# Optimization experiments

Measured on AMD Instinct MI355X. Metric: run time of the kernel, lower is better.

Reference implementation:

```python
import jax, jax.numpy as jnp
import numpy as np

N, E, IN_CH, EDGE_DIM, OUT_CH = 50000, 600000, 128, 64, 128


def setup_inputs() -> dict:
    key = jax.random.key(0)
    ks = jax.random.split(key, 9)
    return {
        "x": jax.random.normal(ks[0], (N, IN_CH), dtype=jnp.float32),
        "edge_index": jax.random.randint(ks[1], (2, E), 0, N, dtype=jnp.int64),
        "edge_attr": jax.random.normal(ks[2], (E, EDGE_DIM), dtype=jnp.float32),
        "Wx": jax.random.normal(ks[3], (IN_CH, OUT_CH), dtype=jnp.float32) * 0.05,
        "bx": jax.random.normal(ks[4], (OUT_CH,), dtype=jnp.float32) * 0.05,
        "We": jax.random.normal(ks[5], (EDGE_DIM, OUT_CH), dtype=jnp.float32) * 0.05,
        "be": jax.random.normal(ks[6], (OUT_CH,), dtype=jnp.float32) * 0.05,
        "Wm": jax.random.normal(ks[7], (2 * OUT_CH, OUT_CH), dtype=jnp.float32) * 0.05,
        "bm": jax.random.normal(ks[8], (OUT_CH,), dtype=jnp.float32) * 0.05,
        "beta": jnp.float32(0.1),
    }


def reference(x, edge_index, edge_attr, Wx, bx, We, be, Wm, bm, beta):
    # node / edge projections
    xp = x @ Wx + bx                      # [N, out]
    ef = edge_attr @ We + be              # [E, out]
    src, dst = edge_index[0], edge_index[1]
    # gather source node features, combine with edge features
    msg = jnp.concatenate([xp[src], ef], axis=1)   # [E, 2*out]
    msg = jax.nn.leaky_relu(msg @ Wm + bm)         # slope 0.01 matches torch default
    # scatter-add into destination nodes
    agg = jax.ops.segment_sum(msg, dst, num_segments=xp.shape[0])  # [N, out]
    return jax.nn.sigmoid(agg) * jax.nn.relu(beta)
```

## Files before the change

kernel.cpp:

```cpp
#include <hip/hip_runtime.h>


#define NB 25000
#define NB_SHIFT 1
#define TPW 4

typedef __bf16 bf16x8 __attribute__((ext_vector_type(8)));
typedef float  f32x4  __attribute__((ext_vector_type(4)));
typedef unsigned short ushort_t;
typedef unsigned int   uint_t;

__device__ __forceinline__ ushort_t f2b(float f) {
    uint_t u = __float_as_uint(f);
    u += 0x7FFF + ((u >> 16) & 1);
    return (ushort_t)(u >> 16);
}
__device__ __forceinline__ uint_t pack2(float a, float b) {
    return (uint_t)f2b(a) | ((uint_t)f2b(b) << 16);
}

__global__ void fuse_weights_kernel(const float* __restrict__ Wx,
                                    const float* __restrict__ bx,
                                    const float* __restrict__ We,
                                    const float* __restrict__ be,
                                    const float* __restrict__ Wm,
                                    const float* __restrict__ bm,
                                    ushort_t* __restrict__ WxmT16,
                                    ushort_t* __restrict__ WemT16,
                                    float* __restrict__ bf) {
    int idx = blockIdx.x * blockDim.x + threadIdx.x;
    if (idx < 128 * 128) {
        int r = idx >> 7, c = idx & 127;
        float acc = 0.f;
        #pragma unroll 8
        for (int j = 0; j < 128; ++j) acc += Wx[r * 128 + j] * Wm[j * 128 + c];
        WxmT16[c * 128 + r] = f2b(acc);
    } else if (idx < 128 * 128 + 64 * 128) {
        int t = idx - 128 * 128;
        int r = t >> 7, c = t & 127;
        float acc = 0.f;
        #pragma unroll 8
        for (int j = 0; j < 128; ++j) acc += We[r * 128 + j] * Wm[(128 + j) * 128 + c];
        WemT16[c * 64 + r] = f2b(acc);
    } else if (idx < 128 * 128 + 64 * 128 + 128) {
        int c = idx - (128 * 128 + 64 * 128);
        float acc = bm[c];
        #pragma unroll 8
        for (int j = 0; j < 128; ++j)
            acc += bx[j] * Wm[j * 128 + c] + be[j] * Wm[(128 + j) * 128 + c];
        bf[c] = acc;
    }
}

__global__ __launch_bounds__(256) void node_gemm_kernel(
        const float* __restrict__ x, const ushort_t* __restrict__ WxmT16,
        const float* __restrict__ bf, ushort_t* __restrict__ ub, int N) {
    int tid = threadIdx.x;
    int g = blockIdx.x * 4 + (tid >> 6);
    if (g >= (N / 16) * 2) return;
    int lane = tid & 63, l15 = lane & 15, quad = lane >> 4;
    int n0 = (g >> 1) * 16;
    int chBase = (g & 1) * 64;

    bf16x8 B[4][4];
    #pragma unroll
    for (int ct = 0; ct < 4; ++ct)
        #pragma unroll
        for (int kk = 0; kk < 4; ++kk)
            B[ct][kk] = __builtin_bit_cast(bf16x8, *((const uint4*)
                &WxmT16[(size_t)(chBase + ct * 16 + l15) * 128 + kk * 32 + quad * 8]));

    bf16x8 A[4];
    #pragma unroll
    for (int kk = 0; kk < 4; ++kk) {
        const float4* s = (const float4*)&x[(size_t)(n0 + l15) * 128 + kk * 32 + quad * 8];
        float4 v0 = s[0], v1 = s[1];
        uint4 w;
        w.x = pack2(v0.x, v0.y);
        w.y = pack2(v0.z, v0.w);
        w.z = pack2(v1.x, v1.y);
        w.w = pack2(v1.z, v1.w);
        A[kk] = __builtin_bit_cast(bf16x8, w);
    }

    f32x4 acc[4] = {{0.f,0.f,0.f,0.f},{0.f,0.f,0.f,0.f},
                    {0.f,0.f,0.f,0.f},{0.f,0.f,0.f,0.f}};
    #pragma unroll
    for (int kk = 0; kk < 4; ++kk)
        #pragma unroll
        for (int ct = 0; ct < 4; ++ct)
            acc[ct] = __builtin_amdgcn_mfma_f32_16x16x32_bf16(B[ct][kk], A[kk], acc[ct], 0, 0, 0);

    #pragma unroll
    for (int ct = 0; ct < 4; ++ct) {
        int ch = chBase + ct * 16 + quad * 4;
        float4 bv = *(const float4*)&bf[ch];
        uint2 w;
        w.x = pack2(acc[ct][0] + bv.x, acc[ct][1] + bv.y);
        w.y = pack2(acc[ct][2] + bv.z, acc[ct][3] + bv.w);
        *((uint2*)&ub[(size_t)(n0 + l15) * 128 + ch]) = w;
    }
}

__global__ __launch_bounds__(1024) void hist_kernel(
        const int* __restrict__ ei, int* __restrict__ cnt, int E) {
    __shared__ int lcnt[NB];
    int t = threadIdx.x;
    for (int i = t; i < NB; i += 1024) lcnt[i] = 0;
    __syncthreads();
    int base = blockIdx.x * 16384;
    #pragma unroll
    for (int j = 0; j < 16; ++j) {
        int e = base + t + j * 1024;
        if (e < E) atomicAdd(&lcnt[ei[E + e] >> NB_SHIFT], 1);
    }
    __syncthreads();
    for (int i = t; i < NB; i += 1024) {
        int c = lcnt[i];
        if (c) atomicAdd(&cnt[i], c);
    }
}

__global__ __launch_bounds__(1024) void scan_kernel(
        const int* __restrict__ cnt, int* __restrict__ start,
        int* __restrict__ cur, int nb, int E) {
    __shared__ int tot[1024];
    int t = threadIdx.x;
    int v[25]; int sum = 0;
    #pragma unroll
    for (int j = 0; j < 25; ++j) {
        int i = t * 25 + j;
        v[j] = (i < nb) ? cnt[i] : 0;
        sum += v[j];
    }
    tot[t] = sum;
    __syncthreads();
    for (int d = 1; d < 1024; d <<= 1) {
        int val = tot[t];
        int add = (t >= d) ? tot[t - d] : 0;
        __syncthreads();
        tot[t] = val + add;
        __syncthreads();
    }
    int ex = (t == 0) ? 0 : tot[t - 1];
    #pragma unroll
    for (int j = 0; j < 25; ++j) {
        int i = t * 25 + j;
        if (i < nb) { start[i] = ex; cur[i] = ex; }
        ex += v[j];
    }
    if (t == 1023) start[nb] = ex;
}

__global__ __launch_bounds__(1024) void binpos_kernel(
        const int* __restrict__ ei, int* __restrict__ cur,
        int* __restrict__ pos, uint_t* __restrict__ recs, int E) {
    __shared__ int lcnt[NB];
    int t = threadIdx.x;
    for (int i = t; i < NB; i += 1024) lcnt[i] = 0;
    __syncthreads();
    int base = blockIdx.x * 16384;
    int myrank[16], mybkt[16];
    #pragma unroll
    for (int j = 0; j < 16; ++j) {
        int e = base + t + j * 1024;
        if (e < E) {
            int b = ei[E + e] >> NB_SHIFT;
            mybkt[j] = b;
            myrank[j] = atomicAdd(&lcnt[b], 1);
        }
    }
    __syncthreads();
    for (int i = t; i < NB; i += 1024) {
        int c = lcnt[i];
        lcnt[i] = c ? atomicAdd(&cur[i], c) : 0;
    }
    __syncthreads();
    #pragma unroll
    for (int j = 0; j < 16; ++j) {
        int e = base + t + j * 1024;
        if (e < E) {
            int p = lcnt[mybkt[j]] + myrank[j];
            pos[e] = p;
            uint_t src  = (uint_t)ei[e];
            uint_t dstl = (uint_t)(ei[E + e] & ((1 << NB_SHIFT) - 1));
            recs[p] = src | (dstl << 16);
        }
    }
}

__global__ __launch_bounds__(256) void msg_stream_kernel(
        const float* __restrict__ ea, const int* __restrict__ pos,
        const ushort_t* __restrict__ WemT16, ushort_t* __restrict__ msgl, int E) {
    int tid = threadIdx.x;
    int g = blockIdx.x * 4 + (tid >> 6);
    int grp = g >> 1;
    int chBase = (g & 1) << 6;
    int t0 = grp * (TPW * 16);
    if (t0 >= E) return;
    int lane = tid & 63, l15 = lane & 15, quad = lane >> 4;

    bf16x8 B[4][2];
    #pragma unroll
    for (int ct = 0; ct < 4; ++ct)
        #pragma unroll
        for (int kk = 0; kk < 2; ++kk)
            B[ct][kk] = __builtin_bit_cast(bf16x8, *((const uint4*)
                &WemT16[(size_t)(chBase + ct * 16 + l15) * 64 + kk * 32 + quad * 8]));

    if (t0 + TPW * 16 <= E) {
        bf16x8 a0[TPW], a1[TPW];
        int pr[TPW];
        #pragma unroll
        for (int tt = 0; tt < TPW; ++tt) {
            int t16 = t0 + tt * 16;
            const float* rowp = &ea[(size_t)(t16 + l15) * 64];
            const float4* sA = (const float4*)(rowp + quad * 8);
            float4 v0 = sA[0], v1 = sA[1];
            uint4 w0;
            w0.x = pack2(v0.x, v0.y);
            w0.y = pack2(v0.z, v0.w);
            w0.z = pack2(v1.x, v1.y);
            w0.w = pack2(v1.z, v1.w);
            a0[tt] = __builtin_bit_cast(bf16x8, w0);
            const float4* sB = (const float4*)(rowp + 32 + quad * 8);
            float4 v2 = sB[0], v3 = sB[1];
            uint4 w1;
            w1.x = pack2(v2.x, v2.y);
            w1.y = pack2(v2.z, v2.w);
            w1.z = pack2(v3.x, v3.y);
            w1.w = pack2(v3.z, v3.w);
            a1[tt] = __builtin_bit_cast(bf16x8, w1);
            pr[tt] = pos[t16 + l15];
        }
        #pragma unroll
        for (int tt = 0; tt < TPW; ++tt) {
            f32x4 acc[4] = {{0.f,0.f,0.f,0.f},{0.f,0.f,0.f,0.f},
                            {0.f,0.f,0.f,0.f},{0.f,0.f,0.f,0.f}};
            #pragma unroll
            for (int ct = 0; ct < 4; ++ct)
                acc[ct] = __builtin_amdgcn_mfma_f32_16x16x32_bf16(B[ct][0], a0[tt], acc[ct], 0, 0, 0);
            #pragma unroll
            for (int ct = 0; ct < 4; ++ct)
                acc[ct] = __builtin_amdgcn_mfma_f32_16x16x32_bf16(B[ct][1], a1[tt], acc[ct], 0, 0, 0);
            #pragma unroll
            for (int ct = 0; ct < 4; ++ct) {
                uint2 w;
                w.x = pack2(acc[ct][0], acc[ct][1]);
                w.y = pack2(acc[ct][2], acc[ct][3]);
                *((uint2*)&msgl[(size_t)pr[tt] * 128 + chBase + ct * 16 + quad * 4]) = w;
            }
        }
    } else {
        for (int tt = 0; tt < TPW; ++tt) {
            int t16 = t0 + tt * 16;
            if (t16 >= E) break;
            const float* rowp = &ea[(size_t)(t16 + l15) * 64];
            const float4* sA = (const float4*)(rowp + quad * 8);
            float4 v0 = sA[0], v1 = sA[1];
            uint4 w0;
            w0.x = pack2(v0.x, v0.y);
            w0.y = pack2(v0.z, v0.w);
            w0.z = pack2(v1.x, v1.y);
            w0.w = pack2(v1.z, v1.w);
            bf16x8 a0 = __builtin_bit_cast(bf16x8, w0);
            const float4* sB = (const float4*)(rowp + 32 + quad * 8);
            float4 v2 = sB[0], v3 = sB[1];
            uint4 w1;
            w1.x = pack2(v2.x, v2.y);
            w1.y = pack2(v2.z, v2.w);
            w1.z = pack2(v3.x, v3.y);
            w1.w = pack2(v3.z, v3.w);
            bf16x8 a1 = __builtin_bit_cast(bf16x8, w1);
            int pr = pos[t16 + l15];

            f32x4 acc[4] = {{0.f,0.f,0.f,0.f},{0.f,0.f,0.f,0.f},
                            {0.f,0.f,0.f,0.f},{0.f,0.f,0.f,0.f}};
            #pragma unroll
            for (int ct = 0; ct < 4; ++ct)
                acc[ct] = __builtin_amdgcn_mfma_f32_16x16x32_bf16(B[ct][0], a0, acc[ct], 0, 0, 0);
            #pragma unroll
            for (int ct = 0; ct < 4; ++ct)
                acc[ct] = __builtin_amdgcn_mfma_f32_16x16x32_bf16(B[ct][1], a1, acc[ct], 0, 0, 0);
            #pragma unroll
            for (int ct = 0; ct < 4; ++ct) {
                uint2 w;
                w.x = pack2(acc[ct][0], acc[ct][1]);
                w.y = pack2(acc[ct][2], acc[ct][3]);
                *((uint2*)&msgl[(size_t)pr * 128 + chBase + ct * 16 + quad * 4]) = w;
            }
        }
    }
}

__global__ __launch_bounds__(256) void segsum_kernel(
        const ushort_t* __restrict__ msgl, const ushort_t* __restrict__ ub,
        const uint_t* __restrict__ recs, const int* __restrict__ start,
        const float* __restrict__ beta, float* __restrict__ out, int N) {
    int wid = blockIdx.x * 4 + (threadIdx.x >> 6);
    if (wid >= NB) return;
    int lane = threadIdx.x & 63;
    int q = lane >> 4;
    int c16 = lane & 15;

    int s0 = start[wid], s1 = start[wid + 1];
    float a0[8] = {0.f,0.f,0.f,0.f,0.f,0.f,0.f,0.f};
    float a1[8] = {0.f,0.f,0.f,0.f,0.f,0.f,0.f,0.f};

    int pA = s0 + q;
    uint_t recA = (pA < s1) ? recs[pA] : 0u;
    int pB = pA + 4;
    uint_t recB = (pB < s1) ? recs[pB] : 0u;

    int pcA = (pA < s1) ? pA : 0;
    uint4 mvA = *(const uint4*)&msgl[(size_t)pcA * 128 + (c16 << 3)];
    uint4 uvA = *(const uint4*)&ub[(size_t)(recA & 0xFFFFu) * 128 + (c16 << 3)];

    while (pA < s1) {
        int pC = pB + 4;
        uint_t recC = (pC < s1) ? recs[pC] : 0u;
        int pcB = (pB < s1) ? pB : pcA;
        uint4 mvB = *(const uint4*)&msgl[(size_t)pcB * 128 + (c16 << 3)];
        uint4 uvB = *(const uint4*)&ub[(size_t)(recB & 0xFFFFu) * 128 + (c16 << 3)];

        float w1 = (recA >> 16) ? 1.f : 0.f;
        float w0 = 1.f - w1;
        {
            float mlo, mhi;
            mlo = __uint_as_float(mvA.x << 16)         + __uint_as_float(uvA.x << 16);
            mhi = __uint_as_float(mvA.x & 0xFFFF0000u) + __uint_as_float(uvA.x & 0xFFFF0000u);
            mlo = fmaxf(mlo, 0.01f * mlo); mhi = fmaxf(mhi, 0.01f * mhi);
            a0[0] += mlo * w0; a1[0] += mlo * w1;
            a0[1] += mhi * w0; a1[1] += mhi * w1;
            mlo = __uint_as_float(mvA.y << 16)         + __uint_as_float(uvA.y << 16);
            mhi = __uint_as_float(mvA.y & 0xFFFF0000u) + __uint_as_float(uvA.y & 0xFFFF0000u);
            mlo = fmaxf(mlo, 0.01f * mlo); mhi = fmaxf(mhi, 0.01f * mhi);
            a0[2] += mlo * w0; a1[2] += mlo * w1;
            a0[3] += mhi * w0; a1[3] += mhi * w1;
            mlo = __uint_as_float(mvA.z << 16)         + __uint_as_float(uvA.z << 16);
            mhi = __uint_as_float(mvA.z & 0xFFFF0000u) + __uint_as_float(uvA.z & 0xFFFF0000u);
            mlo = fmaxf(mlo, 0.01f * mlo); mhi = fmaxf(mhi, 0.01f * mhi);
            a0[4] += mlo * w0; a1[4] += mlo * w1;
            a0[5] += mhi * w0; a1[5] += mhi * w1;
            mlo = __uint_as_float(mvA.w << 16)         + __uint_as_float(uvA.w << 16);
            mhi = __uint_as_float(mvA.w & 0xFFFF0000u) + __uint_as_float(uvA.w & 0xFFFF0000u);
            mlo = fmaxf(mlo, 0.01f * mlo); mhi = fmaxf(mhi, 0.01f * mhi);
            a0[6] += mlo * w0; a1[6] += mlo * w1;
            a0[7] += mhi * w0; a1[7] += mhi * w1;
        }

        pcA = pcB;
        pA = pB; recA = recB; mvA = mvB; uvA = uvB;
        pB = pC; recB = recC;
    }

    #pragma unroll
    for (int j = 0; j < 8; ++j) {
        a0[j] += __shfl_xor(a0[j], 16);
        a0[j] += __shfl_xor(a0[j], 32);
        a1[j] += __shfl_xor(a1[j], 16);
        a1[j] += __shfl_xor(a1[j], 32);
    }

    float rb = beta[0];
    rb = rb > 0.f ? rb : 0.f;
    int h   = lane >> 5;
    int sub = (lane >> 4) & 1;
    int n = (wid << 1) + h;
    if (n < N) {
        float x0, x1, x2, x3;
        if (h == 0) {
            if (sub == 0) { x0 = a0[0]; x1 = a0[1]; x2 = a0[2]; x3 = a0[3]; }
            else          { x0 = a0[4]; x1 = a0[5]; x2 = a0[6]; x3 = a0[7]; }
        } else {
            if (sub == 0) { x0 = a1[0]; x1 = a1[1]; x2 = a1[2]; x3 = a1[3]; }
            else          { x0 = a1[4]; x1 = a1[5]; x2 = a1[6]; x3 = a1[7]; }
        }
        float4 v;
        v.x = rb / (1.f + __expf(-x0));
        v.y = rb / (1.f + __expf(-x1));
        v.z = rb / (1.f + __expf(-x2));
        v.w = rb / (1.f + __expf(-x3));
        ((float4*)out)[(size_t)n * 32 + c16 * 2 + sub] = v;
    }
}

extern "C" void kernel_launch(void* const* d_in, const int* in_sizes, int n_in,
                              void* d_out, int out_size, void* d_ws, size_t ws_size,
                              hipStream_t stream) {
    const float* x    = (const float*)d_in[0];
    const int*   ei   = (const int*)d_in[1];
    const float* ea   = (const float*)d_in[2];
    const float* Wx   = (const float*)d_in[3];
    const float* bx   = (const float*)d_in[4];
    const float* We   = (const float*)d_in[5];
    const float* be   = (const float*)d_in[6];
    const float* Wm   = (const float*)d_in[7];
    const float* bm   = (const float*)d_in[8];
    const float* beta = (const float*)d_in[9];

    int N = in_sizes[0] / 128;
    int E = in_sizes[2] / 64;

    float* out = (float*)d_out;

    char* ws = (char*)d_ws;
    ushort_t* WxmT16 = (ushort_t*)(ws);
    ushort_t* WemT16 = (ushort_t*)(ws + 32768);
    float*    bf     = (float*)(ws + 49152);
    ushort_t* ub     = (ushort_t*)(ws + 65536);
    size_t off = 65536 + (size_t)N * 128 * 2;
    uint_t* recs   = (uint_t*)(ws + off);
    off += (size_t)E * 4;
    int* pos       = (int*)(ws + off);
    off += (size_t)E * 4;
    int* cnt       = (int*)(ws + off);
    int* startb    = (int*)(ws + off + 131072);
    int* cur       = (int*)(ws + off + 262144);
    ushort_t* msgl = (ushort_t*)(ws + off + 393216);

    hipMemsetAsync(cnt, 0, (size_t)NB * sizeof(int), stream);

    fuse_weights_kernel<<<(24704 + 255) / 256, 256, 0, stream>>>(
        Wx, bx, We, be, Wm, bm, WxmT16, WemT16, bf);

    node_gemm_kernel<<<(N / 16 * 2 + 3) / 4, 256, 0, stream>>>(
        x, WxmT16, bf, ub, N);

    int nbBlocks = (E + 16383) / 16384;
    hist_kernel<<<nbBlocks, 1024, 0, stream>>>(ei, cnt, E);
    scan_kernel<<<1, 1024, 0, stream>>>(cnt, startb, cur, NB, E);
    binpos_kernel<<<nbBlocks, 1024, 0, stream>>>(ei, cur, pos, recs, E);

    int ntile  = (E + 15) / 16;
    int ngrp   = (ntile + TPW - 1) / TPW;
    int nwaves = ngrp * 2;
    msg_stream_kernel<<<(nwaves + 3) / 4, 256, 0, stream>>>(
        ea, pos, WemT16, msgl, E);

    segsum_kernel<<<(NB + 3) / 4, 256, 0, stream>>>(
        msgl, ub, recs, startb, beta, out, N);
}
```

Before: 467.7 us.

## Replace LDS-binned sort with global atomics and edge-indexed message layout

The histogram and bin-position kernels drop their 25000-entry shared-memory histograms and 1024-thread blocks, and instead use one global atomic per edge with 256-thread blocks. The pos array is removed. The message kernel now writes each message at its original edge index, so its stores become coalesced instead of scattered. Each sorted record grows to 8 bytes and carries the edge id, so segsum gathers messages indirectly by edge. This trades heavier global atomic contention and a random gather in segsum for removing the large LDS zero/flush passes and the scattered message writes.

```diff
diff --git a/kernel.cpp b/kernel.cpp
--- a/kernel.cpp
+++ b/kernel.cpp
@@ -102,23 +102,10 @@
     }
 }
 
-__global__ __launch_bounds__(1024) void hist_kernel(
+__global__ __launch_bounds__(256) void hist_kernel(
         const int* __restrict__ ei, int* __restrict__ cnt, int E) {
-    __shared__ int lcnt[NB];
-    int t = threadIdx.x;
-    for (int i = t; i < NB; i += 1024) lcnt[i] = 0;
-    __syncthreads();
-    int base = blockIdx.x * 16384;
-    #pragma unroll
-    for (int j = 0; j < 16; ++j) {
-        int e = base + t + j * 1024;
-        if (e < E) atomicAdd(&lcnt[ei[E + e] >> NB_SHIFT], 1);
-    }
-    __syncthreads();
-    for (int i = t; i < NB; i += 1024) {
-        int c = lcnt[i];
-        if (c) atomicAdd(&cnt[i], c);
-    }
+    int e = blockIdx.x * 256 + threadIdx.x;
+    if (e < E) atomicAdd(&cnt[ei[E + e] >> NB_SHIFT], 1);
 }
 
 __global__ __launch_bounds__(1024) void scan_kernel(
@@ -152,45 +139,24 @@
     if (t == 1023) start[nb] = ex;
 }
 
-__global__ __launch_bounds__(1024) void binpos_kernel(
+__global__ __launch_bounds__(256) void binpos_kernel(
         const int* __restrict__ ei, int* __restrict__ cur,
-        int* __restrict__ pos, uint_t* __restrict__ recs, int E) {
-    __shared__ int lcnt[NB];
-    int t = threadIdx.x;
-    for (int i = t; i < NB; i += 1024) lcnt[i] = 0;
-    __syncthreads();
-    int base = blockIdx.x * 16384;
-    int myrank[16], mybkt[16];
-    #pragma unroll
-    for (int j = 0; j < 16; ++j) {
-        int e = base + t + j * 1024;
-        if (e < E) {
-            int b = ei[E + e] >> NB_SHIFT;
-            mybkt[j] = b;
-            myrank[j] = atomicAdd(&lcnt[b], 1);
-        }
-    }
-    __syncthreads();
-    for (int i = t; i < NB; i += 1024) {
-        int c = lcnt[i];
-        lcnt[i] = c ? atomicAdd(&cur[i], c) : 0;
-    }
-    __syncthreads();
-    #pragma unroll
-    for (int j = 0; j < 16; ++j) {
-        int e = base + t + j * 1024;
-        if (e < E) {
-            int p = lcnt[mybkt[j]] + myrank[j];
-            pos[e] = p;
-            uint_t src  = (uint_t)ei[e];
-            uint_t dstl = (uint_t)(ei[E + e] & ((1 << NB_SHIFT) - 1));
-            recs[p] = src | (dstl << 16);
-        }
-    }
+        uint2* __restrict__ rec64, int E) {
+    int e = blockIdx.x * 256 + threadIdx.x;
+    if (e >= E) return;
+    int d = ei[E + e];
+    int b = d >> NB_SHIFT;
+    int p = atomicAdd(&cur[b], 1);
+    uint_t src  = (uint_t)ei[e];
+    uint_t dstl = (uint_t)(d & ((1 << NB_SHIFT) - 1));
+    uint2 r;
+    r.x = src | (dstl << 16);
+    r.y = (uint_t)e;
+    rec64[p] = r;
 }
 
 __global__ __launch_bounds__(256) void msg_stream_kernel(
-        const float* __restrict__ ea, const int* __restrict__ pos,
+        const float* __restrict__ ea,
         const ushort_t* __restrict__ WemT16, ushort_t* __restrict__ msgl, int E) {
     int tid = threadIdx.x;
     int g = blockIdx.x * 4 + (tid >> 6);
@@ -210,7 +176,6 @@
 
     if (t0 + TPW * 16 <= E) {
         bf16x8 a0[TPW], a1[TPW];
-        int pr[TPW];
         #pragma unroll
         for (int tt = 0; tt < TPW; ++tt) {
             int t16 = t0 + tt * 16;
@@ -231,10 +196,10 @@
             w1.z = pack2(v3.x, v3.y);
             w1.w = pack2(v3.z, v3.w);
             a1[tt] = __builtin_bit_cast(bf16x8, w1);
-            pr[tt] = pos[t16 + l15];
         }
         #pragma unroll
         for (int tt = 0; tt < TPW; ++tt) {
+            int t16 = t0 + tt * 16;
             f32x4 acc[4] = {{0.f,0.f,0.f,0.f},{0.f,0.f,0.f,0.f},
                             {0.f,0.f,0.f,0.f},{0.f,0.f,0.f,0.f}};
             #pragma unroll
@@ -248,7 +213,7 @@
                 uint2 w;
                 w.x = pack2(acc[ct][0], acc[ct][1]);
                 w.y = pack2(acc[ct][2], acc[ct][3]);
-                *((uint2*)&msgl[(size_t)pr[tt] * 128 + chBase + ct * 16 + quad * 4]) = w;
+                *((uint2*)&msgl[(size_t)(t16 + l15) * 128 + chBase + ct * 16 + quad * 4]) = w;
             }
         }
     } else {
@@ -272,7 +237,6 @@
             w1.z = pack2(v3.x, v3.y);
             w1.w = pack2(v3.z, v3.w);
             bf16x8 a1 = __builtin_bit_cast(bf16x8, w1);
-            int pr = pos[t16 + l15];
 
             f32x4 acc[4] = {{0.f,0.f,0.f,0.f},{0.f,0.f,0.f,0.f},
                             {0.f,0.f,0.f,0.f},{0.f,0.f,0.f,0.f}};
@@ -287,7 +251,7 @@
                 uint2 w;
                 w.x = pack2(acc[ct][0], acc[ct][1]);
                 w.y = pack2(acc[ct][2], acc[ct][3]);
-                *((uint2*)&msgl[(size_t)pr * 128 + chBase + ct * 16 + quad * 4]) = w;
+                *((uint2*)&msgl[(size_t)(t16 + l15) * 128 + chBase + ct * 16 + quad * 4]) = w;
             }
         }
     }
@@ -295,7 +259,7 @@
 
 __global__ __launch_bounds__(256) void segsum_kernel(
         const ushort_t* __restrict__ msgl, const ushort_t* __restrict__ ub,
-        const uint_t* __restrict__ recs, const int* __restrict__ start,
+        const uint2* __restrict__ rec64, const int* __restrict__ start,
         const float* __restrict__ beta, float* __restrict__ out, int N) {
     int wid = blockIdx.x * 4 + (threadIdx.x >> 6);
     if (wid >= NB) return;
@@ -307,23 +271,22 @@
     float a0[8] = {0.f,0.f,0.f,0.f,0.f,0.f,0.f,0.f};
     float a1[8] = {0.f,0.f,0.f,0.f,0.f,0.f,0.f,0.f};
 
+    uint2 zero; zero.x = 0u; zero.y = 0u;
     int pA = s0 + q;
-    uint_t recA = (pA < s1) ? recs[pA] : 0u;
+    uint2 rA = (pA < s1) ? rec64[pA] : zero;
     int pB = pA + 4;
-    uint_t recB = (pB < s1) ? recs[pB] : 0u;
-
-    int pcA = (pA < s1) ? pA : 0;
-    uint4 mvA = *(const uint4*)&msgl[(size_t)pcA * 128 + (c16 << 3)];
-    uint4 uvA = *(const uint4*)&ub[(size_t)(recA & 0xFFFFu) * 128 + (c16 << 3)];
+    uint2 rB = (pB < s1) ? rec64[pB] : zero;
+
+    uint4 mvA = *(const uint4*)&msgl[(size_t)rA.y * 128 + (c16 << 3)];
+    uint4 uvA = *(const uint4*)&ub[(size_t)(rA.x & 0xFFFFu) * 128 + (c16 << 3)];
 
     while (pA < s1) {
         int pC = pB + 4;
-        uint_t recC = (pC < s1) ? recs[pC] : 0u;
-        int pcB = (pB < s1) ? pB : pcA;
-        uint4 mvB = *(const uint4*)&msgl[(size_t)pcB * 128 + (c16 << 3)];
-        uint4 uvB = *(const uint4*)&ub[(size_t)(recB & 0xFFFFu) * 128 + (c16 << 3)];
-
-        float w1 = (recA >> 16) ? 1.f : 0.f;
+        uint2 rC = (pC < s1) ? rec64[pC] : zero;
+        uint4 mvB = *(const uint4*)&msgl[(size_t)rB.y * 128 + (c16 << 3)];
+        uint4 uvB = *(const uint4*)&ub[(size_t)(rB.x & 0xFFFFu) * 128 + (c16 << 3)];
+
+        float w1 = (rA.x >> 16) ? 1.f : 0.f;
         float w0 = 1.f - w1;
         {
             float mlo, mhi;
@@ -349,9 +312,8 @@
             a0[7] += mhi * w0; a1[7] += mhi * w1;
         }
 
-        pcA = pcB;
-        pA = pB; recA = recB; mvA = mvB; uvA = uvB;
-        pB = pC; recB = recC;
+        pA = pB; rA = rB; mvA = mvB; uvA = uvB;
+        pB = pC; rB = rC;
     }
 
     #pragma unroll
@@ -410,10 +372,8 @@
     float*    bf     = (float*)(ws + 49152);
     ushort_t* ub     = (ushort_t*)(ws + 65536);
     size_t off = 65536 + (size_t)N * 128 * 2;
-    uint_t* recs   = (uint_t*)(ws + off);
-    off += (size_t)E * 4;
-    int* pos       = (int*)(ws + off);
-    off += (size_t)E * 4;
+    uint2* rec64   = (uint2*)(ws + off);
+    off += (size_t)E * 8;
     int* cnt       = (int*)(ws + off);
     int* startb    = (int*)(ws + off + 131072);
     int* cur       = (int*)(ws + off + 262144);
@@ -427,17 +387,17 @@
     node_gemm_kernel<<<(N / 16 * 2 + 3) / 4, 256, 0, stream>>>(
         x, WxmT16, bf, ub, N);
 
-    int nbBlocks = (E + 16383) / 16384;
-    hist_kernel<<<nbBlocks, 1024, 0, stream>>>(ei, cnt, E);
+    int ebBlocks = (E + 255) / 256;
+    hist_kernel<<<ebBlocks, 256, 0, stream>>>(ei, cnt, E);
     scan_kernel<<<1, 1024, 0, stream>>>(cnt, startb, cur, NB, E);
-    binpos_kernel<<<nbBlocks, 1024, 0, stream>>>(ei, cur, pos, recs, E);
+    binpos_kernel<<<ebBlocks, 256, 0, stream>>>(ei, cur, rec64, E);
 
     int ntile  = (E + 15) / 16;
     int ngrp   = (ntile + TPW - 1) / TPW;
     int nwaves = ngrp * 2;
     msg_stream_kernel<<<(nwaves + 3) / 4, 256, 0, stream>>>(
-        ea, pos, WemT16, msgl, E);
+        ea, WemT16, msgl, E);
 
     segsum_kernel<<<(NB + 3) / 4, 256, 0, stream>>>(
-        msgl, ub, recs, startb, beta, out, N);
-}
+        msgl, ub, rec64, startb, beta, out, N);
+}
```

New measurement: 475.7 us. About the same (+1.7%).
